# Optimization experiments

Measured on AMD Instinct MI355X. Metric: run time of the kernel, lower is better.

## Reference

```python
import jax, jax.numpy as jnp
import numpy as np

B, N, C = 2, 100000, 256
H, D, S = 8, 64, 64
INNER = H * D

def setup_inputs() -> dict:
    key = jax.random.key(0)
    ks = jax.random.split(key, 5)
    x = jax.random.normal(ks[0], (B, N, C), dtype=jnp.float32)
    W_x = jax.random.normal(ks[1], (C, INNER), dtype=jnp.float32) / np.sqrt(C)
    b_x = jnp.zeros((INNER,), dtype=jnp.float32)
    W_fx = jax.random.normal(ks[2], (C, INNER), dtype=jnp.float32) / np.sqrt(C)
    b_fx = jnp.zeros((INNER,), dtype=jnp.float32)
    W_slice = jax.random.normal(ks[3], (D, S), dtype=jnp.float32) / np.sqrt(D)
    b_slice = jnp.zeros((S,), dtype=jnp.float32)
    temperature = jnp.ones((1, 1, H, 1), dtype=jnp.float32) * 0.5
    return {"x": x, "W_x": W_x, "b_x": b_x, "W_fx": W_fx, "b_fx": b_fx,
            "W_slice": W_slice, "b_slice": b_slice, "temperature": temperature}

def reference(x, W_x, b_x, W_fx, b_fx, W_slice, b_slice, temperature):
    b, n, _ = x.shape
    # linear projections to (B, N, H, D)
    px = (x @ W_x + b_x).reshape(b, n, H, D)   # query-like projection
    fx = (x @ W_fx + b_fx).reshape(b, n, H, D) # feature (value) projection
    # slice logits (B, N, H, S)
    slice_proj = jnp.einsum('bnhd,ds->bnhs', px, W_slice) + b_slice
    temp = jnp.clip(temperature, 0.1, 5.0)     # (1,1,H,1), broadcast over S
    slice_weights = jax.nn.softmax(slice_proj / temp, axis=-1)  # (B,N,H,S)
    slice_norm = slice_weights.sum(axis=1)     # (B,H,S)
    # weighted aggregation of tokens into slice tokens (B,H,S,D)
    slice_token = jnp.einsum('bnhs,bnhd->bhsd', slice_weights, fx)
    slice_token = slice_token / (slice_norm[..., None] + 1e-5)
    return slice_token
```

## Files before the change

### kernel.cpp

```cpp
#include <hip/hip_runtime.h>
#include <hip/hip_bf16.h>
#include <cstdint>

#define B_     2
#define N_     100000
#define C_     256
#define H_     8
#define D_     64
#define S_     64
#define INNER_ 512

#define TILE_T 64
#define NTILES ((N_ + TILE_T - 1) / TILE_T)
#define PBLK   32

#define WEFFT_OFF 0
#define WFXT_OFF  262144
#define BIASE_OFF 524288
#define ACC_OFF   526336
#define NRM_OFF   788480
#define WS_END    792576

typedef __attribute__((ext_vector_type(8))) short short8;
typedef __attribute__((ext_vector_type(4))) float f32x4;

__device__ inline short f2bf(float f) {
    __hip_bfloat16 h = __float2bfloat16(f);
    short s; __builtin_memcpy(&s, &h, 2); return s;
}
__device__ inline uint32_t pk2(float a, float b) {
    __hip_bfloat162 h = __float22bfloat162_rn(float2{a, b});
    uint32_t u; __builtin_memcpy(&u, &h, 4); return u;
}

__global__ void prep_kernel(const float* __restrict__ W_x,
                            const float* __restrict__ b_x,
                            const float* __restrict__ W_fx,
                            const float* __restrict__ W_slice,
                            const float* __restrict__ b_slice,
                            uint8_t* __restrict__ wsb) {
    int id = blockIdx.x * 256 + threadIdx.x;
    const int NW = H_ * S_ * C_;
    if (id < NW) {
        int k = id & 255, s = (id >> 8) & 63, h = id >> 14;
        float a = 0.f;
        #pragma unroll 8
        for (int d = 0; d < D_; ++d)
            a = fmaf(W_x[k * INNER_ + h * 64 + d], W_slice[d * 64 + s], a);
        ((short*)(wsb + WEFFT_OFF))[(h * 64 + s) * 256 + k] = f2bf(a);
    } else if (id < 2 * NW) {
        int j = id - NW;
        int k = j & 255, d = (j >> 8) & 63, h = j >> 14;
        ((short*)(wsb + WFXT_OFF))[(h * 64 + d) * 256 + k] =
            f2bf(W_fx[k * INNER_ + h * 64 + d]);
    } else if (id < 2 * NW + H_ * S_) {
        int j = id - 2 * NW;
        int s = j & 63, h = j >> 6;
        float a = 0.f;
        #pragma unroll 8
        for (int d = 0; d < D_; ++d)
            a = fmaf(b_x[h * 64 + d], W_slice[d * 64 + s], a);
        ((float*)(wsb + BIASE_OFF))[h * 64 + s] = a + b_slice[s];
    }
}

__global__ __launch_bounds__(256, 2) void main_kernel(
        const float* __restrict__ x,
        const float* __restrict__ b_fx,
        const float* __restrict__ temperature,
        const uint8_t* __restrict__ wsb,
        float* __restrict__ accg,
        float* __restrict__ nrmg) {
    __shared__ short xs[TILE_T * 264];
    __shared__ short wsl[S_ * 72];
    __shared__ short fsl[D_ * 72];
    __shared__ float smA[2 * TILE_T];
    __shared__ float smB[2 * TILE_T];

    const int tid  = threadIdx.x;
    const int p = blockIdx.x, h = blockIdx.y, b = blockIdx.z;
    const int lane = tid & 63, wv = tid >> 6;
    const int l = lane & 15, q = lane >> 4;
    const int g = wv & 1, nh = wv >> 1;

    const short* wT = (const short*)(wsb + (g ? WFXT_OFF : WEFFT_OFF)) + h * (64 * 256);
    short8 breg[2][8];
    #pragma unroll
    for (int nt = 0; nt < 2; ++nt)
        #pragma unroll
        for (int k = 0; k < 8; ++k)
            breg[nt][k] = *(const short8*)(wT + (nh * 32 + nt * 16 + l) * 256 + k * 32 + q * 8);

    float invt; { float t = temperature[h]; t = fminf(fmaxf(t, 0.1f), 5.0f); invt = 1.f / t; }
    float bias_n[2];
    #pragma unroll
    for (int nt = 0; nt < 2; ++nt) {
        int n = nh * 32 + nt * 16 + l;
        bias_n[nt] = g ? b_fx[h * 64 + n] : ((const float*)(wsb + BIASE_OFF))[h * 64 + n];
    }

    const float* xb = x + (size_t)b * ((size_t)N_ * C_);
    f32x4 accO[4] = {};
    float nrmacc[2] = {0.f, 0.f};

    for (int tile = p; tile < NTILES; tile += PBLK) {
        const int t0 = tile * TILE_T;
        __syncthreads();

        {
            int tok = tid & 63, kq = tid >> 6;
            int gt = t0 + tok;
            const float* src = xb + (size_t)gt * C_ + kq * 64;
            short* dst = xs + tok * 264 + kq * 64;
            if (gt < N_) {
                #pragma unroll
                for (int i = 0; i < 8; ++i) {
                    float4 f0 = *(const float4*)(src + i * 8);
                    float4 f1 = *(const float4*)(src + i * 8 + 4);
                    uint32_t u[4] = { pk2(f0.x, f0.y), pk2(f0.z, f0.w),
                                      pk2(f1.x, f1.y), pk2(f1.z, f1.w) };
                    *(int4*)(dst + i * 8) = *(int4*)u;
                }
            } else {
                int4 z = make_int4(0, 0, 0, 0);
                #pragma unroll
                for (int i = 0; i < 8; ++i) *(int4*)(dst + i * 8) = z;
            }
        }
        __syncthreads();

        f32x4 acc[4][2] = {};
        #pragma unroll
        for (int k = 0; k < 8; ++k) {
            short8 a[4];
            #pragma unroll
            for (int m = 0; m < 4; ++m)
                a[m] = *(const short8*)(xs + (m * 16 + l) * 264 + k * 32 + q * 8);
            #pragma unroll
            for (int m = 0; m < 4; ++m)
                #pragma unroll
                for (int nt = 0; nt < 2; ++nt)
                    acc[m][nt] = __builtin_amdgcn_mfma_f32_16x16x32_bf16(
                        a[m], breg[nt][k], acc[m][nt], 0, 0, 0);
        }

        float pm[4][4], ps[4][4];
        if (g == 0) {
            #pragma unroll
            for (int m = 0; m < 4; ++m)
                #pragma unroll
                for (int nt = 0; nt < 2; ++nt)
                    #pragma unroll
                    for (int r = 0; r < 4; ++r)
                        acc[m][nt][r] = (acc[m][nt][r] + bias_n[nt]) * invt;
            #pragma unroll
            for (int m = 0; m < 4; ++m)
                #pragma unroll
                for (int r = 0; r < 4; ++r) {
                    float v = fmaxf(acc[m][0][r], acc[m][1][r]);
                    v = fmaxf(v, __shfl_xor(v, 1, 64));
                    v = fmaxf(v, __shfl_xor(v, 2, 64));
                    v = fmaxf(v, __shfl_xor(v, 4, 64));
                    v = fmaxf(v, __shfl_xor(v, 8, 64));
                    pm[m][r] = v;
                }
            if (l == 0)
                #pragma unroll
                for (int m = 0; m < 4; ++m)
                    #pragma unroll
                    for (int r = 0; r < 4; ++r)
                        smA[nh * 64 + m * 16 + q * 4 + r] = pm[m][r];
        } else {
            #pragma unroll
            for (int m = 0; m < 4; ++m)
                #pragma unroll
                for (int nt = 0; nt < 2; ++nt) {
                    int dd = nh * 32 + nt * 16 + l, tt = m * 16 + q * 4;
                    *(uint32_t*)(fsl + dd * 72 + tt) =
                        pk2(acc[m][nt][0] + bias_n[nt], acc[m][nt][1] + bias_n[nt]);
                    *(uint32_t*)(fsl + dd * 72 + tt + 2) =
                        pk2(acc[m][nt][2] + bias_n[nt], acc[m][nt][3] + bias_n[nt]);
                }
        }
        __syncthreads();

        if (g == 0) {
            #pragma unroll
            for (int m = 0; m < 4; ++m)
                #pragma unroll
                for (int r = 0; r < 4; ++r) {
                    float Mx = fmaxf(pm[m][r], smA[(1 - nh) * 64 + m * 16 + q * 4 + r]);
                    acc[m][0][r] = __expf(acc[m][0][r] - Mx);
                    acc[m][1][r] = __expf(acc[m][1][r] - Mx);
                    float sv = acc[m][0][r] + acc[m][1][r];
                    sv += __shfl_xor(sv, 1, 64);
                    sv += __shfl_xor(sv, 2, 64);
                    sv += __shfl_xor(sv, 4, 64);
                    sv += __shfl_xor(sv, 8, 64);
                    ps[m][r] = sv;
                }
            if (l == 0)
                #pragma unroll
                for (int m = 0; m < 4; ++m)
                    #pragma unroll
                    for (int r = 0; r < 4; ++r)
                        smB[nh * 64 + m * 16 + q * 4 + r] = ps[m][r];
        }
        __syncthreads();

        if (g == 0) {
            #pragma unroll
            for (int m = 0; m < 4; ++m) {
                #pragma unroll
                for (int r = 0; r < 4; ++r) {
                    float Sv = ps[m][r] + smB[(1 - nh) * 64 + m * 16 + q * 4 + r];
                    float rs = __builtin_amdgcn_rcpf(Sv);
                    int gt = t0 + m * 16 + q * 4 + r;
                    float w0 = acc[m][0][r] * rs, w1 = acc[m][1][r] * rs;
                    if (gt >= N_) { w0 = 0.f; w1 = 0.f; }
                    acc[m][0][r] = w0; acc[m][1][r] = w1;
                    nrmacc[0] += w0; nrmacc[1] += w1;
                }
                #pragma unroll
                for (int nt = 0; nt < 2; ++nt) {
                    int ss = nh * 32 + nt * 16 + l, tt = m * 16 + q * 4;
                    *(uint32_t*)(wsl + ss * 72 + tt)     = pk2(acc[m][nt][0], acc[m][nt][1]);
                    *(uint32_t*)(wsl + ss * 72 + tt + 2) = pk2(acc[m][nt][2], acc[m][nt][3]);
                }
            }
        }
        __syncthreads();

        #pragma unroll
        for (int kk = 0; kk < 2; ++kk) {
            short8 aw = *(const short8*)(wsl + (wv * 16 + l) * 72 + kk * 32 + q * 8);
            #pragma unroll
            for (int nt = 0; nt < 4; ++nt) {
                short8 bf = *(const short8*)(fsl + (nt * 16 + l) * 72 + kk * 32 + q * 8);
                accO[nt] = __builtin_amdgcn_mfma_f32_16x16x32_bf16(aw, bf, accO[nt], 0, 0, 0);
            }
        }
    }

    float* ag = accg + (size_t)((b * H_ + h) * 64) * 64;
    #pragma unroll
    for (int nt = 0; nt < 4; ++nt)
        #pragma unroll
        for (int r = 0; r < 4; ++r)
            atomicAdd(ag + (wv * 16 + q * 4 + r) * 64 + nt * 16 + l, accO[nt][r]);
    if (g == 0) {
        #pragma unroll
        for (int nt = 0; nt < 2; ++nt) {
            float v = nrmacc[nt];
            v += __shfl_xor(v, 16, 64);
            v += __shfl_xor(v, 32, 64);
            if (lane < 16)
                atomicAdd(nrmg + (b * H_ + h) * 64 + nh * 32 + nt * 16 + lane, v);
        }
    }
}

__global__ void finalize_kernel(const uint8_t* __restrict__ wsb, float* __restrict__ out) {
    int idx = blockIdx.x * blockDim.x + threadIdx.x;
    float a = ((const float*)(wsb + ACC_OFF))[idx];
    float n = ((const float*)(wsb + NRM_OFF))[idx / D_];
    out[idx] = a / (n + 1e-5f);
}

extern "C" void kernel_launch(void* const* d_in, const int* in_sizes, int n_in,
                              void* d_out, int out_size, void* d_ws, size_t ws_size,
                              hipStream_t stream) {
    const float* x           = (const float*)d_in[0];
    const float* W_x         = (const float*)d_in[1];
    const float* b_x         = (const float*)d_in[2];
    const float* W_fx        = (const float*)d_in[3];
    const float* b_fx        = (const float*)d_in[4];
    const float* W_slice     = (const float*)d_in[5];
    const float* b_slice     = (const float*)d_in[6];
    const float* temperature = (const float*)d_in[7];
    float* out = (float*)d_out;
    uint8_t* wsb = (uint8_t*)d_ws;

    hipMemsetAsync(wsb + ACC_OFF, 0, (NRM_OFF - ACC_OFF) + B_ * H_ * S_ * 4, stream);

    int prep_threads = 2 * H_ * S_ * C_ + H_ * S_;
    prep_kernel<<<dim3((prep_threads + 255) / 256), dim3(256), 0, stream>>>(
        W_x, b_x, W_fx, W_slice, b_slice, wsb);

    main_kernel<<<dim3(PBLK, H_, B_), dim3(256), 0, stream>>>(
        x, b_fx, temperature, wsb,
        (float*)(wsb + ACC_OFF), (float*)(wsb + NRM_OFF));

    finalize_kernel<<<dim3((B_ * H_ * S_ * D_) / 256), dim3(256), 0, stream>>>(wsb, out);
}
```

Before: 663.8 us.

## Double grid, merge softmax syncs, union LDS, and reduce partials via slabs

Doubles the token-split block count and raises launch bounds to four blocks per SM. The shared tiles are unioned so LDS use per block shrinks. The two-pass softmax cross-wave max/sum exchange is merged into one barrier using rescaled partial sums. The x tile load is rewritten so each wave reads a contiguous row. When the workspace is large enough, atomics and the memset are replaced with per-block slab writes plus a reduction kernel. The prep kernel is also reorganised per wave. Risks are register pressure at the higher occupancy and extra traffic for the slab reduction.

```diff
diff --git a/kernel.cpp b/kernel.cpp
--- a/kernel.cpp
+++ b/kernel.cpp
@@ -12,14 +12,17 @@
 
 #define TILE_T 64
 #define NTILES ((N_ + TILE_T - 1) / TILE_T)
-#define PBLK   32
+#define PBLK   64
 
 #define WEFFT_OFF 0
 #define WFXT_OFF  262144
 #define BIASE_OFF 524288
 #define ACC_OFF   526336
 #define NRM_OFF   788480
-#define WS_END    792576
+#define WS_SMALL_END 792576
+#define SLAB_OFF  526336
+#define NSLAB_OFF (SLAB_OFF + 16777216)
+#define WS_BIG_END (NSLAB_OFF + 262144)
 
 typedef __attribute__((ext_vector_type(8))) short short8;
 typedef __attribute__((ext_vector_type(4))) float f32x4;
@@ -39,41 +42,43 @@
                             const float* __restrict__ W_slice,
                             const float* __restrict__ b_slice,
                             uint8_t* __restrict__ wsb) {
-    int id = blockIdx.x * 256 + threadIdx.x;
-    const int NW = H_ * S_ * C_;
-    if (id < NW) {
-        int k = id & 255, s = (id >> 8) & 63, h = id >> 14;
+    int wid  = (blockIdx.x * 256 + threadIdx.x) >> 6;
+    int lane = threadIdx.x & 63;
+    if (wid < H_ * C_) {
+        int h = wid >> 8, k = wid & 255;
+        const float* wx = W_x + k * INNER_ + h * 64;
         float a = 0.f;
         #pragma unroll 8
         for (int d = 0; d < D_; ++d)
-            a = fmaf(W_x[k * INNER_ + h * 64 + d], W_slice[d * 64 + s], a);
-        ((short*)(wsb + WEFFT_OFF))[(h * 64 + s) * 256 + k] = f2bf(a);
-    } else if (id < 2 * NW) {
-        int j = id - NW;
-        int k = j & 255, d = (j >> 8) & 63, h = j >> 14;
-        ((short*)(wsb + WFXT_OFF))[(h * 64 + d) * 256 + k] =
-            f2bf(W_fx[k * INNER_ + h * 64 + d]);
-    } else if (id < 2 * NW + H_ * S_) {
-        int j = id - 2 * NW;
-        int s = j & 63, h = j >> 6;
+            a = fmaf(wx[d], W_slice[d * 64 + lane], a);
+        ((short*)(wsb + WEFFT_OFF))[(h * 64 + lane) * 256 + k] = f2bf(a);
+    } else if (wid < 2 * H_ * C_) {
+        int j = wid - H_ * C_;
+        int h = j >> 8, k = j & 255;
+        ((short*)(wsb + WFXT_OFF))[(h * 64 + lane) * 256 + k] =
+            f2bf(W_fx[k * INNER_ + h * 64 + lane]);
+    } else if (wid < 2 * H_ * C_ + H_) {
+        int h = wid - 2 * H_ * C_;
         float a = 0.f;
         #pragma unroll 8
         for (int d = 0; d < D_; ++d)
-            a = fmaf(b_x[h * 64 + d], W_slice[d * 64 + s], a);
-        ((float*)(wsb + BIASE_OFF))[h * 64 + s] = a + b_slice[s];
-    }
-}
-
-__global__ __launch_bounds__(256, 2) void main_kernel(
+            a = fmaf(b_x[h * 64 + d], W_slice[d * 64 + lane], a);
+        ((float*)(wsb + BIASE_OFF))[h * 64 + lane] = a + b_slice[lane];
+    }
+}
+
+template<bool SLAB>
+__global__ __launch_bounds__(256, 4) void main_kernel(
         const float* __restrict__ x,
         const float* __restrict__ b_fx,
         const float* __restrict__ temperature,
         const uint8_t* __restrict__ wsb,
         float* __restrict__ accg,
         float* __restrict__ nrmg) {
-    __shared__ short xs[TILE_T * 264];
-    __shared__ short wsl[S_ * 72];
-    __shared__ short fsl[D_ * 72];
+    __shared__ union {
+        short xs[TILE_T * 264];
+        struct { short wsl[S_ * 72]; short fsl[D_ * 72]; } wf;
+    } u;
     __shared__ float smA[2 * TILE_T];
     __shared__ float smB[2 * TILE_T];
 
@@ -108,23 +113,19 @@
         __syncthreads();
 
         {
-            int tok = tid & 63, kq = tid >> 6;
-            int gt = t0 + tok;
-            const float* src = xb + (size_t)gt * C_ + kq * 64;
-            short* dst = xs + tok * 264 + kq * 64;
-            if (gt < N_) {
-                #pragma unroll
-                for (int i = 0; i < 8; ++i) {
-                    float4 f0 = *(const float4*)(src + i * 8);
-                    float4 f1 = *(const float4*)(src + i * 8 + 4);
-                    uint32_t u[4] = { pk2(f0.x, f0.y), pk2(f0.z, f0.w),
-                                      pk2(f1.x, f1.y), pk2(f1.z, f1.w) };
-                    *(int4*)(dst + i * 8) = *(int4*)u;
-                }
-            } else {
-                int4 z = make_int4(0, 0, 0, 0);
-                #pragma unroll
-                for (int i = 0; i < 8; ++i) *(int4*)(dst + i * 8) = z;
+            const int col = lane * 4;
+            #pragma unroll 8
+            for (int j = 0; j < 16; ++j) {
+                int row = wv + 4 * j;
+                int gt = t0 + row;
+                short* dst = u.xs + row * 264 + col;
+                if (gt < N_) {
+                    float4 v = *(const float4*)(xb + (size_t)gt * C_ + col);
+                    uint2 pk = { pk2(v.x, v.y), pk2(v.z, v.w) };
+                    *(uint2*)dst = pk;
+                } else {
+                    *(uint2*)dst = uint2{0u, 0u};
+                }
             }
         }
         __syncthreads();
@@ -135,7 +136,7 @@
             short8 a[4];
             #pragma unroll
             for (int m = 0; m < 4; ++m)
-                a[m] = *(const short8*)(xs + (m * 16 + l) * 264 + k * 32 + q * 8);
+                a[m] = *(const short8*)(u.xs + (m * 16 + l) * 264 + k * 32 + q * 8);
             #pragma unroll
             for (int m = 0; m < 4; ++m)
                 #pragma unroll
@@ -144,67 +145,31 @@
                         a[m], breg[nt][k], acc[m][nt], 0, 0, 0);
         }
 
-        float pm[4][4], ps[4][4];
         if (g == 0) {
             #pragma unroll
             for (int m = 0; m < 4; ++m)
                 #pragma unroll
-                for (int nt = 0; nt < 2; ++nt)
-                    #pragma unroll
-                    for (int r = 0; r < 4; ++r)
-                        acc[m][nt][r] = (acc[m][nt][r] + bias_n[nt]) * invt;
-            #pragma unroll
-            for (int m = 0; m < 4; ++m)
-                #pragma unroll
                 for (int r = 0; r < 4; ++r) {
-                    float v = fmaxf(acc[m][0][r], acc[m][1][r]);
-                    v = fmaxf(v, __shfl_xor(v, 1, 64));
-                    v = fmaxf(v, __shfl_xor(v, 2, 64));
-                    v = fmaxf(v, __shfl_xor(v, 4, 64));
-                    v = fmaxf(v, __shfl_xor(v, 8, 64));
-                    pm[m][r] = v;
-                }
-            if (l == 0)
-                #pragma unroll
-                for (int m = 0; m < 4; ++m)
-                    #pragma unroll
-                    for (int r = 0; r < 4; ++r)
-                        smA[nh * 64 + m * 16 + q * 4 + r] = pm[m][r];
-        } else {
-            #pragma unroll
-            for (int m = 0; m < 4; ++m)
-                #pragma unroll
-                for (int nt = 0; nt < 2; ++nt) {
-                    int dd = nh * 32 + nt * 16 + l, tt = m * 16 + q * 4;
-                    *(uint32_t*)(fsl + dd * 72 + tt) =
-                        pk2(acc[m][nt][0] + bias_n[nt], acc[m][nt][1] + bias_n[nt]);
-                    *(uint32_t*)(fsl + dd * 72 + tt + 2) =
-                        pk2(acc[m][nt][2] + bias_n[nt], acc[m][nt][3] + bias_n[nt]);
-                }
-        }
-        __syncthreads();
-
-        if (g == 0) {
-            #pragma unroll
-            for (int m = 0; m < 4; ++m)
-                #pragma unroll
-                for (int r = 0; r < 4; ++r) {
-                    float Mx = fmaxf(pm[m][r], smA[(1 - nh) * 64 + m * 16 + q * 4 + r]);
-                    acc[m][0][r] = __expf(acc[m][0][r] - Mx);
-                    acc[m][1][r] = __expf(acc[m][1][r] - Mx);
-                    float sv = acc[m][0][r] + acc[m][1][r];
+                    float v0 = (acc[m][0][r] + bias_n[0]) * invt;
+                    float v1 = (acc[m][1][r] + bias_n[1]) * invt;
+                    float mx = fmaxf(v0, v1);
+                    mx = fmaxf(mx, __shfl_xor(mx, 1, 64));
+                    mx = fmaxf(mx, __shfl_xor(mx, 2, 64));
+                    mx = fmaxf(mx, __shfl_xor(mx, 4, 64));
+                    mx = fmaxf(mx, __shfl_xor(mx, 8, 64));
+                    float e0 = __expf(v0 - mx), e1 = __expf(v1 - mx);
+                    acc[m][0][r] = e0; acc[m][1][r] = e1;
+                    float sv = e0 + e1;
                     sv += __shfl_xor(sv, 1, 64);
                     sv += __shfl_xor(sv, 2, 64);
                     sv += __shfl_xor(sv, 4, 64);
                     sv += __shfl_xor(sv, 8, 64);
-                    ps[m][r] = sv;
-                }
-            if (l == 0)
-                #pragma unroll
-                for (int m = 0; m < 4; ++m)
-                    #pragma unroll
-                    for (int r = 0; r < 4; ++r)
-                        smB[nh * 64 + m * 16 + q * 4 + r] = ps[m][r];
+                    if (l == 0) {
+                        int tok = m * 16 + q * 4 + r;
+                        smA[nh * 64 + tok] = mx;
+                        smB[nh * 64 + tok] = sv;
+                    }
+                }
         }
         __syncthreads();
 
@@ -213,55 +178,102 @@
             for (int m = 0; m < 4; ++m) {
                 #pragma unroll
                 for (int r = 0; r < 4; ++r) {
-                    float Sv = ps[m][r] + smB[(1 - nh) * 64 + m * 16 + q * 4 + r];
-                    float rs = __builtin_amdgcn_rcpf(Sv);
-                    int gt = t0 + m * 16 + q * 4 + r;
-                    float w0 = acc[m][0][r] * rs, w1 = acc[m][1][r] * rs;
-                    if (gt >= N_) { w0 = 0.f; w1 = 0.f; }
+                    int tok = m * 16 + q * 4 + r;
+                    float p0 = smA[tok], p1 = smA[64 + tok];
+                    float s0 = smB[tok], s1 = smB[64 + tok];
+                    float M  = fmaxf(p0, p1);
+                    float c0 = __expf(p0 - M), c1 = __expf(p1 - M);
+                    float S  = fmaf(s0, c0, s1 * c1);
+                    float f  = (nh ? c1 : c0) * __builtin_amdgcn_rcpf(S);
+                    if (t0 + tok >= N_) f = 0.f;
+                    float w0 = acc[m][0][r] * f, w1 = acc[m][1][r] * f;
+                    nrmacc[0] += w0; nrmacc[1] += w1;
                     acc[m][0][r] = w0; acc[m][1][r] = w1;
-                    nrmacc[0] += w0; nrmacc[1] += w1;
                 }
                 #pragma unroll
                 for (int nt = 0; nt < 2; ++nt) {
                     int ss = nh * 32 + nt * 16 + l, tt = m * 16 + q * 4;
-                    *(uint32_t*)(wsl + ss * 72 + tt)     = pk2(acc[m][nt][0], acc[m][nt][1]);
-                    *(uint32_t*)(wsl + ss * 72 + tt + 2) = pk2(acc[m][nt][2], acc[m][nt][3]);
-                }
-            }
+                    uint2 pk = { pk2(acc[m][nt][0], acc[m][nt][1]),
+                                 pk2(acc[m][nt][2], acc[m][nt][3]) };
+                    *(uint2*)(u.wf.wsl + ss * 72 + tt) = pk;
+                }
+            }
+        } else {
+            #pragma unroll
+            for (int m = 0; m < 4; ++m)
+                #pragma unroll
+                for (int nt = 0; nt < 2; ++nt) {
+                    int dd = nh * 32 + nt * 16 + l, tt = m * 16 + q * 4;
+                    uint2 pk = { pk2(acc[m][nt][0] + bias_n[nt], acc[m][nt][1] + bias_n[nt]),
+                                 pk2(acc[m][nt][2] + bias_n[nt], acc[m][nt][3] + bias_n[nt]) };
+                    *(uint2*)(u.wf.fsl + dd * 72 + tt) = pk;
+                }
         }
         __syncthreads();
 
         #pragma unroll
         for (int kk = 0; kk < 2; ++kk) {
-            short8 aw = *(const short8*)(wsl + (wv * 16 + l) * 72 + kk * 32 + q * 8);
+            short8 aw = *(const short8*)(u.wf.wsl + (wv * 16 + l) * 72 + kk * 32 + q * 8);
             #pragma unroll
             for (int nt = 0; nt < 4; ++nt) {
-                short8 bf = *(const short8*)(fsl + (nt * 16 + l) * 72 + kk * 32 + q * 8);
+                short8 bf = *(const short8*)(u.wf.fsl + (nt * 16 + l) * 72 + kk * 32 + q * 8);
                 accO[nt] = __builtin_amdgcn_mfma_f32_16x16x32_bf16(aw, bf, accO[nt], 0, 0, 0);
             }
         }
     }
 
-    float* ag = accg + (size_t)((b * H_ + h) * 64) * 64;
-    #pragma unroll
-    for (int nt = 0; nt < 4; ++nt)
-        #pragma unroll
-        for (int r = 0; r < 4; ++r)
-            atomicAdd(ag + (wv * 16 + q * 4 + r) * 64 + nt * 16 + l, accO[nt][r]);
-    if (g == 0) {
-        #pragma unroll
-        for (int nt = 0; nt < 2; ++nt) {
-            float v = nrmacc[nt];
-            v += __shfl_xor(v, 16, 64);
-            v += __shfl_xor(v, 32, 64);
-            if (lane < 16)
-                atomicAdd(nrmg + (b * H_ + h) * 64 + nh * 32 + nt * 16 + lane, v);
-        }
-    }
-}
-
-__global__ void finalize_kernel(const uint8_t* __restrict__ wsb, float* __restrict__ out) {
-    int idx = blockIdx.x * blockDim.x + threadIdx.x;
+    if (SLAB) {
+        float* sp = accg + ((size_t)(b * H_ + h) * PBLK + p) * 4096;
+        #pragma unroll
+        for (int nt = 0; nt < 4; ++nt)
+            #pragma unroll
+            for (int r = 0; r < 4; ++r)
+                sp[(wv * 16 + q * 4 + r) * 64 + nt * 16 + l] = accO[nt][r];
+        if (g == 0) {
+            #pragma unroll
+            for (int nt = 0; nt < 2; ++nt) {
+                float v = nrmacc[nt];
+                v += __shfl_xor(v, 16, 64);
+                v += __shfl_xor(v, 32, 64);
+                if (lane < 16)
+                    nrmg[((b * H_ + h) * PBLK + p) * 64 + nh * 32 + nt * 16 + lane] = v;
+            }
+        }
+    } else {
+        float* ag = accg + (size_t)((b * H_ + h) * 64) * 64;
+        #pragma unroll
+        for (int nt = 0; nt < 4; ++nt)
+            #pragma unroll
+            for (int r = 0; r < 4; ++r)
+                atomicAdd(ag + (wv * 16 + q * 4 + r) * 64 + nt * 16 + l, accO[nt][r]);
+        if (g == 0) {
+            #pragma unroll
+            for (int nt = 0; nt < 2; ++nt) {
+                float v = nrmacc[nt];
+                v += __shfl_xor(v, 16, 64);
+                v += __shfl_xor(v, 32, 64);
+                if (lane < 16)
+                    atomicAdd(nrmg + (b * H_ + h) * 64 + nh * 32 + nt * 16 + lane, v);
+            }
+        }
+    }
+}
+
+__global__ void finalize_big(const float* __restrict__ slab,
+                             const float* __restrict__ nslab,
+                             float* __restrict__ out) {
+    int idx = blockIdx.x * 256 + threadIdx.x;
+    int bh = idx >> 12, sd = idx & 4095, s = sd >> 6;
+    const float* sp = slab  + (size_t)bh * PBLK * 4096 + sd;
+    const float* np = nslab + bh * PBLK * 64 + s;
+    float acc = 0.f, nn = 0.f;
+    #pragma unroll 8
+    for (int p = 0; p < PBLK; ++p) { acc += sp[p * 4096]; nn += np[p * 64]; }
+    out[idx] = acc / (nn + 1e-5f);
+}
+
+__global__ void finalize_small(const uint8_t* __restrict__ wsb, float* __restrict__ out) {
+    int idx = blockIdx.x * 256 + threadIdx.x;
     float a = ((const float*)(wsb + ACC_OFF))[idx];
     float n = ((const float*)(wsb + NRM_OFF))[idx / D_];
     out[idx] = a / (n + 1e-5f);
@@ -281,15 +293,21 @@
     float* out = (float*)d_out;
     uint8_t* wsb = (uint8_t*)d_ws;
 
-    hipMemsetAsync(wsb + ACC_OFF, 0, (NRM_OFF - ACC_OFF) + B_ * H_ * S_ * 4, stream);
-
-    int prep_threads = 2 * H_ * S_ * C_ + H_ * S_;
-    prep_kernel<<<dim3((prep_threads + 255) / 256), dim3(256), 0, stream>>>(
+    int prep_waves = 2 * H_ * C_ + H_;
+    prep_kernel<<<dim3((prep_waves + 3) / 4), dim3(256), 0, stream>>>(
         W_x, b_x, W_fx, W_slice, b_slice, wsb);
 
-    main_kernel<<<dim3(PBLK, H_, B_), dim3(256), 0, stream>>>(
-        x, b_fx, temperature, wsb,
-        (float*)(wsb + ACC_OFF), (float*)(wsb + NRM_OFF));
-
-    finalize_kernel<<<dim3((B_ * H_ * S_ * D_) / 256), dim3(256), 0, stream>>>(wsb, out);
-}
+    if (ws_size >= (size_t)WS_BIG_END) {
+        main_kernel<true><<<dim3(PBLK, H_, B_), dim3(256), 0, stream>>>(
+            x, b_fx, temperature, wsb,
+            (float*)(wsb + SLAB_OFF), (float*)(wsb + NSLAB_OFF));
+        finalize_big<<<dim3(256), dim3(256), 0, stream>>>(
+            (const float*)(wsb + SLAB_OFF), (const float*)(wsb + NSLAB_OFF), out);
+    } else {
+        hipMemsetAsync(wsb + ACC_OFF, 0, (NRM_OFF - ACC_OFF) + B_ * H_ * S_ * 4, stream);
+        main_kernel<false><<<dim3(PBLK, H_, B_), dim3(256), 0, stream>>>(
+            x, b_fx, temperature, wsb,
+            (float*)(wsb + ACC_OFF), (float*)(wsb + NRM_OFF));
+        finalize_small<<<dim3(256), dim3(256), 0, stream>>>(wsb, out);
+    }
+}
```

Measured after the change: 734.3 us. 10.6% more time.
